# Kernel tuning notes

Measured on AMD Instinct MI355X. Metric: run time of the kernel, lower is better.

## Reference

```python
import jax, jax.numpy as jnp
import numpy as np

EMBED_DIM = 1024
HEAD_DIM = 128

def setup_inputs() -> dict:
    key = jax.random.key(0)
    ks = jax.random.split(key, 7)
    B, S = 4, 2048
    x = jax.random.normal(ks[0], (B, S, EMBED_DIM), dtype=jnp.float32)
    # Linear params: weight [embed_dim, head_dim] (applied as x @ W + b), scaled init
    scale = 1.0 / np.sqrt(EMBED_DIM)
    Wq = jax.random.normal(ks[1], (EMBED_DIM, HEAD_DIM), dtype=jnp.float32) * scale
    Wk = jax.random.normal(ks[2], (EMBED_DIM, HEAD_DIM), dtype=jnp.float32) * scale
    Wv = jax.random.normal(ks[3], (EMBED_DIM, HEAD_DIM), dtype=jnp.float32) * scale
    bq = jax.random.normal(ks[4], (HEAD_DIM,), dtype=jnp.float32) * 0.01
    bk = jax.random.normal(ks[5], (HEAD_DIM,), dtype=jnp.float32) * 0.01
    bv = jax.random.normal(ks[6], (HEAD_DIM,), dtype=jnp.float32) * 0.01
    return {"x": x, "Wq": Wq, "bq": bq, "Wk": Wk, "bk": bk, "Wv": Wv, "bv": bv}

def reference(x, Wq, bq, Wk, bk, Wv, bv):
    # x: [B, S, E]
    S = x.shape[1]
    norm = jnp.asarray(HEAD_DIM ** 0.5, x.dtype)
    q = x @ Wq + bq  # [B, S, D]
    k = x @ Wk + bk
    v = x @ Wv + bv
    scores = jnp.einsum('bsd,btd->bst', q, k) / norm  # [B, S, S]
    causal = jnp.tril(jnp.ones((S, S), dtype=bool))
    scores = jnp.where(causal, scores, -jnp.inf)
    att = jax.nn.softmax(scores, axis=-1)
    return jnp.einsum('bst,btd->bsd', att, v)  # [B, S, D]
```

## Files before the change

kernel.cpp:

```cpp
#include <hip/hip_runtime.h>
#include <hip/hip_bf16.h>

typedef __attribute__((ext_vector_type(8))) short short8;
typedef __attribute__((ext_vector_type(4))) float f32x4;

static __device__ __forceinline__ unsigned short f2bf(float f){
  union { float f; unsigned int u; } v; v.f = f;
  unsigned int r = v.u + 0x7fffu + ((v.u >> 16) & 1u);
  return (unsigned short)(r >> 16);
}
static __device__ __forceinline__ float bf2f(unsigned short u){
  union { unsigned int u; float f; } v; v.u = ((unsigned int)u) << 16; return v.f;
}

static __device__ __forceinline__ void load_lds16(const unsigned short* g, unsigned short* l){
  __builtin_amdgcn_global_load_lds(
      (const __attribute__((address_space(1))) unsigned int*)(g),
      (__attribute__((address_space(3))) unsigned int*)(l), 16, 0, 0);
}

__global__ void k_cvt_x(const float* __restrict__ x, unsigned short* __restrict__ xb){
  int i = (blockIdx.x * 256 + threadIdx.x) * 8;
  float4 a = *(const float4*)(x + i);
  float4 b = *(const float4*)(x + i + 4);
  unsigned short h[8];
  h[0]=f2bf(a.x); h[1]=f2bf(a.y); h[2]=f2bf(a.z); h[3]=f2bf(a.w);
  h[4]=f2bf(b.x); h[5]=f2bf(b.y); h[6]=f2bf(b.z); h[7]=f2bf(b.w);
  *(uint4*)(xb + i) = *(uint4*)h;
}

__global__ void k_prep_w(const float* __restrict__ Wq, const float* __restrict__ Wk,
                         const float* __restrict__ Wv,
                         const float* __restrict__ bq, const float* __restrict__ bk,
                         const float* __restrict__ bv,
                         unsigned short* __restrict__ Wt, float* __restrict__ bias){
  int gid = blockIdx.x * 256 + threadIdx.x;
  int p = gid >> 17;
  int rem = gid & 131071;
  int d = rem >> 10, e = rem & 1023;
  const float* W = (p==0) ? Wq : ((p==1) ? Wk : Wv);
  Wt[gid] = f2bf(W[e*128 + d]);
  if (gid < 384){
    int pp = gid >> 7, dd = gid & 127;
    bias[gid] = (pp==0) ? bq[dd] : ((pp==1) ? bk[dd] : bv[dd]);
  }
}

__global__ __launch_bounds__(256) void k_gemm_qkv(
    const unsigned short* __restrict__ Xb, const unsigned short* __restrict__ Wt,
    const float* __restrict__ bias,
    unsigned short* __restrict__ Qsw, unsigned short* __restrict__ Ksw,
    unsigned short* __restrict__ Vsw){
  __shared__ __align__(16) unsigned short As[64*64];
  __shared__ __align__(16) unsigned short Bs[128*64];
  int tid = threadIdx.x;
  int m0 = blockIdx.x * 64;
  int p  = blockIdx.y;
  int w = tid >> 6, lane = tid & 63, quad = lane >> 4, l16 = lane & 15;
  int wm = (w & 1) * 32, wn = (w >> 1) * 64;
  f32x4 acc[2][4];
  #pragma unroll
  for (int i=0;i<2;i++)
    #pragma unroll
    for (int j=0;j<4;j++) acc[i][j] = (f32x4){0.f,0.f,0.f,0.f};

  const unsigned short* Wp = Wt + p * (128*1024);
  const unsigned short* Ag = Xb + (m0 + w*16 + (lane>>3))*1024 + (lane&7)*8;
  const unsigned short* Bg = Wp + (w*32 + (lane>>3))*1024 + (lane&7)*8;
  unsigned short* Al = As + w*16*64;
  unsigned short* Bl = Bs + w*32*64;

  for (int k0 = 0; k0 < 1024; k0 += 64){
    load_lds16(Ag + k0,        Al);
    load_lds16(Ag + k0 + 8192, Al + 512);
    #pragma unroll
    for (int s=0; s<4; s++)
      load_lds16(Bg + k0 + s*8192, Bl + s*512);
    __syncthreads();
    #pragma unroll
    for (int kk=0; kk<64; kk+=32){
      short8 af[2], bf[4];
      #pragma unroll
      for (int i=0;i<2;i++) af[i] = *(const short8*)(As + (wm + i*16 + l16)*64 + kk + quad*8);
      #pragma unroll
      for (int j=0;j<4;j++) bf[j] = *(const short8*)(Bs + (wn + j*16 + l16)*64 + kk + quad*8);
      #pragma unroll
      for (int i=0;i<2;i++)
        #pragma unroll
        for (int j=0;j<4;j++)
          acc[i][j] = __builtin_amdgcn_mfma_f32_16x16x32_bf16(af[i], bf[j], acc[i][j], 0,0,0);
    }
    __syncthreads();
  }
  const float qscale = 0.08838834764831845f;
  if (p < 2){
    unsigned short* dst = (p==0)? Qsw : Ksw;
    float scale = (p==0)? qscale : 1.0f;
    #pragma unroll
    for (int i=0;i<2;i++){
      #pragma unroll
      for (int j=0;j<4;j++){
        int col = wn + j*16 + l16;
        float bv_ = bias[p*128 + col];
        int kc = col >> 5, q2 = (col >> 3) & 3, jj = col & 7;
        #pragma unroll
        for (int r=0;r<4;r++){
          int row = m0 + wm + i*16 + quad*4 + r;
          int rt = row >> 4, m = row & 15;
          dst[rt*2048 + kc*512 + q2*128 + m*8 + jj] = f2bf((acc[i][j][r] + bv_)*scale);
        }
      }
    }
  } else {
    #pragma unroll
    for (int i=0;i<2;i++){
      int row0 = m0 + wm + i*16 + quad*4;
      int bb = row0 >> 11, s = row0 & 2047;
      int t64 = s >> 6, srem = s & 63;
      int kc2 = srem >> 5, q2v = (srem >> 3) & 3, jjb = srem & 7;
      #pragma unroll
      for (int j=0;j<4;j++){
        int col = wn + j*16 + l16;
        float bv_ = bias[256 + col];
        int nt = (wn + j*16) >> 4;
        unsigned short pk[4];
        #pragma unroll
        for (int r=0;r<4;r++) pk[r] = f2bf(acc[i][j][r] + bv_);
        *(uint2*)(Vsw + (bb*32+t64)*8192 + nt*1024 + kc2*512 + q2v*128 + l16*8 + jjb) = *(uint2*)pk;
      }
    }
  }
}

__global__ __launch_bounds__(64) void k_attn(
    const unsigned short* __restrict__ Qsw, const unsigned short* __restrict__ Ksw,
    const unsigned short* __restrict__ Vsw, unsigned short* __restrict__ Apart){
  __shared__ __align__(16) unsigned short Pw[2*16*80];
  int x = blockIdx.x;
  int b = x & 3;
  int t = x >> 2;
  int c = t & 7;
  int qb = 63 - (t >> 3);
  int T32 = (qb >> 1) + 1;
  int nch = (T32 + 3) >> 2;
  if (c >= nch) return;
  int lane = threadIdx.x;
  int quad = lane >> 4, l16 = lane & 15;
  int q0 = qb * 32;

  short8 aq[2][4];
  #pragma unroll
  for (int s=0;s<2;s++)
    #pragma unroll
    for (int kc=0;kc<4;kc++)
      aq[s][kc] = *(const short8*)(Qsw + (b*128 + qb*2 + s)*2048 + kc*512 + lane*8);

  f32x4 o[2][8];
  #pragma unroll
  for (int s=0;s<2;s++)
    #pragma unroll
    for (int i=0;i<8;i++) o[s][i] = (f32x4){0.f,0.f,0.f,0.f};
  float mcol[2] = {-1e30f,-1e30f};
  float lcol[2] = {0.f,0.f};
  short8 ap[2][2];

  const unsigned short* Kb = Ksw + b*128*2048;
  const unsigned short* Vb = Vsw + b*32*8192;

  int tEnd = (T32 < c*4+4) ? T32 : (c*4+4);
  for (int tt = c*4; tt < tEnd; tt++){
    int t0 = tt * 64;
    f32x4 sc[2][4];
    #pragma unroll
    for (int s=0;s<2;s++)
      #pragma unroll
      for (int nt=0;nt<4;nt++) sc[s][nt] = (f32x4){0.f,0.f,0.f,0.f};
    #pragma unroll
    for (int nt=0;nt<4;nt++){
      const unsigned short* Kt = Kb + ((t0>>4)+nt)*2048 + lane*8;
      #pragma unroll
      for (int kc=0;kc<4;kc++){
        short8 kf = *(const short8*)(Kt + kc*512);
        sc[0][nt] = __builtin_amdgcn_mfma_f32_16x16x32_bf16(kf, aq[0][kc], sc[0][nt], 0,0,0);
        sc[1][nt] = __builtin_amdgcn_mfma_f32_16x16x32_bf16(kf, aq[1][kc], sc[1][nt], 0,0,0);
      }
    }
    #pragma unroll
    for (int s=0;s<2;s++){
      int qs = q0 + s*16;
      if (t0 + 63 > qs){
        #pragma unroll
        for (int nt=0;nt<4;nt++){
          int kb_ = t0 + nt*16 + quad*4;
          #pragma unroll
          for (int r=0;r<4;r++)
            if (kb_ + r > qs + l16) sc[s][nt][r] = -1e30f;
        }
      }
      float mt_ = -1e30f;
      #pragma unroll
      for (int nt=0;nt<4;nt++)
        #pragma unroll
        for (int r=0;r<4;r++) mt_ = fmaxf(mt_, sc[s][nt][r]);
      mt_ = fmaxf(mt_, __shfl_xor(mt_, 16));
      mt_ = fmaxf(mt_, __shfl_xor(mt_, 32));
      float mn = fmaxf(mcol[s], mt_);
      float al = __expf(mcol[s] - mn);
      mcol[s] = mn;
      float ls = 0.f;
      #pragma unroll
      for (int nt=0;nt<4;nt++)
        #pragma unroll
        for (int r=0;r<4;r++){
          float pv = __expf(sc[s][nt][r] - mn);
          sc[s][nt][r] = pv;
          ls += pv;
        }
      ls += __shfl_xor(ls, 16);
      ls += __shfl_xor(ls, 32);
      lcol[s] = lcol[s]*al + ls;
      #pragma unroll
      for (int r=0;r<4;r++){
        float ar = __shfl(al, quad*4 + r);
        #pragma unroll
        for (int nt=0;nt<8;nt++) o[s][nt][r] *= ar;
      }
      unsigned short* Pws = Pw + s*1280;
      #pragma unroll
      for (int nt=0;nt<4;nt++){
        unsigned short pk[4];
        #pragma unroll
        for (int r=0;r<4;r++) pk[r] = f2bf(sc[s][nt][r]);
        *(uint2*)(Pws + l16*80 + nt*16 + quad*4) = *(uint2*)pk;
      }
      ap[s][0] = *(const short8*)(Pws + l16*80 + quad*8);
      ap[s][1] = *(const short8*)(Pws + l16*80 + 32 + quad*8);
    }
    const unsigned short* Vt0 = Vb + (t0>>6)*8192 + lane*8;
    #pragma unroll
    for (int nt=0; nt<8; nt++)
      #pragma unroll
      for (int kc2=0;kc2<2;kc2++){
        short8 vf = *(const short8*)(Vt0 + nt*1024 + kc2*512);
        o[0][nt] = __builtin_amdgcn_mfma_f32_16x16x32_bf16(ap[0][kc2], vf, o[0][nt], 0,0,0);
        o[1][nt] = __builtin_amdgcn_mfma_f32_16x16x32_bf16(ap[1][kc2], vf, o[1][nt], 0,0,0);
      }
  }

  unsigned short* slot = Apart + (size_t)(((b*64 + qb)*8 + c)) * 4224;
  #pragma unroll
  for (int s=0;s<2;s++)
    #pragma unroll
    for (int nt=0;nt<8;nt++){
      unsigned short pk[4];
      #pragma unroll
      for (int r=0;r<4;r++) pk[r] = f2bf(o[s][nt][r]);
      *(uint2*)(slot + (s*8+nt)*256 + lane*4) = *(uint2*)pk;
    }
  float* fslot = (float*)(slot + 4096);
  if (quad == 0){
    #pragma unroll
    for (int s=0;s<2;s++){
      fslot[s*16 + l16]      = mcol[s];
      fslot[32 + s*16 + l16] = lcol[s];
    }
  }
}

__global__ __launch_bounds__(256) void k_acomb(const unsigned short* __restrict__ Apart,
                                               float* __restrict__ out){
  int b = blockIdx.x & 3, qb = blockIdx.x >> 2;
  int T32 = (qb >> 1) + 1;
  int nch = (T32 + 3) >> 2;
  const unsigned short* slot0 = Apart + (size_t)((b*64 + qb)*8) * 4224;
  int tid = threadIdx.x;
  int row = tid >> 3;
  int c0 = (tid & 7) * 16;
  int s = row >> 4, qrow = row & 15;
  int quad = qrow >> 2, r = qrow & 3;
  int nt = c0 >> 4;
  float m = -1e30f;
  for (int c=0;c<nch;c++){
    const float* fs = (const float*)(slot0 + c*4224 + 4096);
    m = fmaxf(m, fs[s*16 + qrow]);
  }
  float acc[16];
  #pragma unroll
  for (int k=0;k<16;k++) acc[k] = 0.f;
  float lsum = 0.f;
  for (int c=0;c<nch;c++){
    const float* fs = (const float*)(slot0 + c*4224 + 4096);
    float e = __expf(fs[s*16 + qrow] - m);
    lsum += fs[32 + s*16 + qrow] * e;
    const unsigned short* ob = slot0 + c*4224 + (s*8+nt)*256 + quad*64 + r;
    #pragma unroll
    for (int k=0;k<16;k++)
      acc[k] += bf2f(ob[k*4]) * e;
  }
  float inv = 1.0f / lsum;
  float* op = out + (size_t)(b*2048 + qb*32 + row)*128 + c0;
  #pragma unroll
  for (int g=0;g<4;g++){
    float4 rv = {acc[g*4]*inv, acc[g*4+1]*inv, acc[g*4+2]*inv, acc[g*4+3]*inv};
    *(float4*)(op + g*4) = rv;
  }
}

extern "C" void kernel_launch(void* const* d_in, const int* in_sizes, int n_in,
                              void* d_out, int out_size, void* d_ws, size_t ws_size,
                              hipStream_t stream) {
  const float* x  = (const float*)d_in[0];
  const float* Wq = (const float*)d_in[1];
  const float* bq = (const float*)d_in[2];
  const float* Wk = (const float*)d_in[3];
  const float* bk = (const float*)d_in[4];
  const float* Wv = (const float*)d_in[5];
  const float* bv = (const float*)d_in[6];
  char* ws = (char*)d_ws;
  unsigned short* Xb   = (unsigned short*)(ws);
  unsigned short* Wt   = (unsigned short*)(ws + 16777216);
  float*          bias = (float*)(ws + 17563648);
  unsigned short* Qsw  = (unsigned short*)(ws + 17565184);
  unsigned short* Ksw  = (unsigned short*)(ws + 19662336);
  unsigned short* Vsw  = (unsigned short*)(ws + 21759488);
  unsigned short* Apart= (unsigned short*)(ws + 23856640);
  float* out = (float*)d_out;

  hipLaunchKernelGGL(k_cvt_x,   dim3(4096),    dim3(256), 0, stream, x, Xb);
  hipLaunchKernelGGL(k_prep_w,  dim3(1536),    dim3(256), 0, stream, Wq, Wk, Wv, bq, bk, bv, Wt, bias);
  hipLaunchKernelGGL(k_gemm_qkv,dim3(128,3),   dim3(256), 0, stream, Xb, Wt, bias, Qsw, Ksw, Vsw);
  hipLaunchKernelGGL(k_attn,    dim3(2048),    dim3(64),  0, stream, Qsw, Ksw, Vsw, Apart);
  hipLaunchKernelGGL(k_acomb,   dim3(256),     dim3(256), 0, stream, Apart, out);
}
```

Before: 141.6 us.

## Merge prep kernels, enlarge QKV GEMM tile, and fold log2e into Q scale

The two preprocessing kernels (x to bf16, weight transpose and bias) are merged into one launch, which removes one kernel launch and its drain gap. The QKV GEMM tile grows from 64 to 128 rows per block, so each wave computes a 64x64 output, raising data reuse per LDS load but halving the grid to 192 blocks on a 256-CU device. Log2(e) is folded into the Q scale so the softmax and combine paths can use exp2f instead of __expf. The net effect of the smaller grid against the better reuse is uncertain.

After: 144.1 us. Within noise of the previous version (+1.8%).

```diff
diff --git a/kernel.cpp b/kernel.cpp
--- a/kernel.cpp
+++ b/kernel.cpp
@@ -19,30 +19,31 @@
       (__attribute__((address_space(3))) unsigned int*)(l), 16, 0, 0);
 }
 
-__global__ void k_cvt_x(const float* __restrict__ x, unsigned short* __restrict__ xb){
-  int i = (blockIdx.x * 256 + threadIdx.x) * 8;
-  float4 a = *(const float4*)(x + i);
-  float4 b = *(const float4*)(x + i + 4);
-  unsigned short h[8];
-  h[0]=f2bf(a.x); h[1]=f2bf(a.y); h[2]=f2bf(a.z); h[3]=f2bf(a.w);
-  h[4]=f2bf(b.x); h[5]=f2bf(b.y); h[6]=f2bf(b.z); h[7]=f2bf(b.w);
-  *(uint4*)(xb + i) = *(uint4*)h;
-}
-
-__global__ void k_prep_w(const float* __restrict__ Wq, const float* __restrict__ Wk,
-                         const float* __restrict__ Wv,
-                         const float* __restrict__ bq, const float* __restrict__ bk,
-                         const float* __restrict__ bv,
-                         unsigned short* __restrict__ Wt, float* __restrict__ bias){
-  int gid = blockIdx.x * 256 + threadIdx.x;
-  int p = gid >> 17;
-  int rem = gid & 131071;
-  int d = rem >> 10, e = rem & 1023;
-  const float* W = (p==0) ? Wq : ((p==1) ? Wk : Wv);
-  Wt[gid] = f2bf(W[e*128 + d]);
-  if (gid < 384){
-    int pp = gid >> 7, dd = gid & 127;
-    bias[gid] = (pp==0) ? bq[dd] : ((pp==1) ? bk[dd] : bv[dd]);
+__global__ void k_prep(const float* __restrict__ x, unsigned short* __restrict__ xb,
+                       const float* __restrict__ Wq, const float* __restrict__ Wk,
+                       const float* __restrict__ Wv,
+                       const float* __restrict__ bq, const float* __restrict__ bk,
+                       const float* __restrict__ bv,
+                       unsigned short* __restrict__ Wt, float* __restrict__ bias){
+  if (blockIdx.x < 4096){
+    int i = (blockIdx.x * 256 + threadIdx.x) * 8;
+    float4 a = *(const float4*)(x + i);
+    float4 b = *(const float4*)(x + i + 4);
+    unsigned short h[8];
+    h[0]=f2bf(a.x); h[1]=f2bf(a.y); h[2]=f2bf(a.z); h[3]=f2bf(a.w);
+    h[4]=f2bf(b.x); h[5]=f2bf(b.y); h[6]=f2bf(b.z); h[7]=f2bf(b.w);
+    *(uint4*)(xb + i) = *(uint4*)h;
+  } else {
+    int gid = (blockIdx.x - 4096) * 256 + threadIdx.x;
+    int p = gid >> 17;
+    int rem = gid & 131071;
+    int d = rem >> 10, e = rem & 1023;
+    const float* W = (p==0) ? Wq : ((p==1) ? Wk : Wv);
+    Wt[gid] = f2bf(W[e*128 + d]);
+    if (gid < 384){
+      int pp = gid >> 7, dd = gid & 127;
+      bias[gid] = (pp==0) ? bq[dd] : ((pp==1) ? bk[dd] : bv[dd]);
+    }
   }
 }
 
@@ -51,53 +52,54 @@
     const float* __restrict__ bias,
     unsigned short* __restrict__ Qsw, unsigned short* __restrict__ Ksw,
     unsigned short* __restrict__ Vsw){
-  __shared__ __align__(16) unsigned short As[64*64];
+  __shared__ __align__(16) unsigned short As[128*64];
   __shared__ __align__(16) unsigned short Bs[128*64];
   int tid = threadIdx.x;
-  int m0 = blockIdx.x * 64;
+  int m0 = blockIdx.x * 128;
   int p  = blockIdx.y;
   int w = tid >> 6, lane = tid & 63, quad = lane >> 4, l16 = lane & 15;
-  int wm = (w & 1) * 32, wn = (w >> 1) * 64;
-  f32x4 acc[2][4];
-  #pragma unroll
-  for (int i=0;i<2;i++)
+  int wm = (w >> 1) * 64, wn = (w & 1) * 64;
+  f32x4 acc[4][4];
+  #pragma unroll
+  for (int i=0;i<4;i++)
     #pragma unroll
     for (int j=0;j<4;j++) acc[i][j] = (f32x4){0.f,0.f,0.f,0.f};
 
   const unsigned short* Wp = Wt + p * (128*1024);
-  const unsigned short* Ag = Xb + (m0 + w*16 + (lane>>3))*1024 + (lane&7)*8;
-  const unsigned short* Bg = Wp + (w*32 + (lane>>3))*1024 + (lane&7)*8;
-  unsigned short* Al = As + w*16*64;
-  unsigned short* Bl = Bs + w*32*64;
+  int rowbase = w * 32;
+  const unsigned short* Ag = Xb + (m0 + rowbase + (lane>>3))*1024 + (lane&7)*8;
+  const unsigned short* Bg = Wp + (rowbase + (lane>>3))*1024 + (lane&7)*8;
+  unsigned short* Al = As + rowbase*64;
+  unsigned short* Bl = Bs + rowbase*64;
 
   for (int k0 = 0; k0 < 1024; k0 += 64){
-    load_lds16(Ag + k0,        Al);
-    load_lds16(Ag + k0 + 8192, Al + 512);
-    #pragma unroll
-    for (int s=0; s<4; s++)
-      load_lds16(Bg + k0 + s*8192, Bl + s*512);
+    #pragma unroll
+    for (int s8=0; s8<4; s8++){
+      load_lds16(Ag + k0 + s8*8192, Al + s8*512);
+      load_lds16(Bg + k0 + s8*8192, Bl + s8*512);
+    }
     __syncthreads();
     #pragma unroll
     for (int kk=0; kk<64; kk+=32){
-      short8 af[2], bf[4];
-      #pragma unroll
-      for (int i=0;i<2;i++) af[i] = *(const short8*)(As + (wm + i*16 + l16)*64 + kk + quad*8);
+      short8 af[4], bf[4];
+      #pragma unroll
+      for (int i=0;i<4;i++) af[i] = *(const short8*)(As + (wm + i*16 + l16)*64 + kk + quad*8);
       #pragma unroll
       for (int j=0;j<4;j++) bf[j] = *(const short8*)(Bs + (wn + j*16 + l16)*64 + kk + quad*8);
       #pragma unroll
-      for (int i=0;i<2;i++)
+      for (int i=0;i<4;i++)
         #pragma unroll
         for (int j=0;j<4;j++)
           acc[i][j] = __builtin_amdgcn_mfma_f32_16x16x32_bf16(af[i], bf[j], acc[i][j], 0,0,0);
     }
     __syncthreads();
   }
-  const float qscale = 0.08838834764831845f;
+  const float qscale = 0.08838834764831845f * 1.44269504088896340f;
   if (p < 2){
     unsigned short* dst = (p==0)? Qsw : Ksw;
     float scale = (p==0)? qscale : 1.0f;
     #pragma unroll
-    for (int i=0;i<2;i++){
+    for (int i=0;i<4;i++){
       #pragma unroll
       for (int j=0;j<4;j++){
         int col = wn + j*16 + l16;
@@ -113,7 +115,7 @@
     }
   } else {
     #pragma unroll
-    for (int i=0;i<2;i++){
+    for (int i=0;i<4;i++){
       int row0 = m0 + wm + i*16 + quad*4;
       int bb = row0 >> 11, s = row0 & 2047;
       int t64 = s >> 6, srem = s & 63;
@@ -205,14 +207,14 @@
       mt_ = fmaxf(mt_, __shfl_xor(mt_, 16));
       mt_ = fmaxf(mt_, __shfl_xor(mt_, 32));
       float mn = fmaxf(mcol[s], mt_);
-      float al = __expf(mcol[s] - mn);
+      float al = exp2f(mcol[s] - mn);
       mcol[s] = mn;
       float ls = 0.f;
       #pragma unroll
       for (int nt=0;nt<4;nt++)
         #pragma unroll
         for (int r=0;r<4;r++){
-          float pv = __expf(sc[s][nt][r] - mn);
+          float pv = exp2f(sc[s][nt][r] - mn);
           sc[s][nt][r] = pv;
           ls += pv;
         }
@@ -290,7 +292,7 @@
   float lsum = 0.f;
   for (int c=0;c<nch;c++){
     const float* fs = (const float*)(slot0 + c*4224 + 4096);
-    float e = __expf(fs[s*16 + qrow] - m);
+    float e = exp2f(fs[s*16 + qrow] - m);
     lsum += fs[32 + s*16 + qrow] * e;
     const unsigned short* ob = slot0 + c*4224 + (s*8+nt)*256 + quad*64 + r;
     #pragma unroll
@@ -326,9 +328,8 @@
   unsigned short* Apart= (unsigned short*)(ws + 23856640);
   float* out = (float*)d_out;
 
-  hipLaunchKernelGGL(k_cvt_x,   dim3(4096),    dim3(256), 0, stream, x, Xb);
-  hipLaunchKernelGGL(k_prep_w,  dim3(1536),    dim3(256), 0, stream, Wq, Wk, Wv, bq, bk, bv, Wt, bias);
-  hipLaunchKernelGGL(k_gemm_qkv,dim3(128,3),   dim3(256), 0, stream, Xb, Wt, bias, Qsw, Ksw, Vsw);
-  hipLaunchKernelGGL(k_attn,    dim3(2048),    dim3(64),  0, stream, Qsw, Ksw, Vsw, Apart);
-  hipLaunchKernelGGL(k_acomb,   dim3(256),     dim3(256), 0, stream, Apart, out);
-}
+  hipLaunchKernelGGL(k_prep,    dim3(5632),  dim3(256), 0, stream, x, Xb, Wq, Wk, Wv, bq, bk, bv, Wt, bias);
+  hipLaunchKernelGGL(k_gemm_qkv,dim3(64,3),  dim3(256), 0, stream, Xb, Wt, bias, Qsw, Ksw, Vsw);
+  hipLaunchKernelGGL(k_attn,    dim3(2048),  dim3(64),  0, stream, Qsw, Ksw, Vsw, Apart);
+  hipLaunchKernelGGL(k_acomb,   dim3(256),   dim3(256), 0, stream, Apart, out);
+}
```
